# Kernel tuning notes

Measured on AMD Instinct MI355X. Metric: run time of the kernel, lower is better.

The kernel has to match this reference:

```python
import jax, jax.numpy as jnp
import numpy as np

N_NODES = 16384   # n_features in the torch code (graph nodes)
N_EDGES = 262144  # nnz of sparse Laplacian (avg degree 16)
K = 4             # receptive_field_k (Chebyshev order)
F_OUT = 32        # gconv_filter_size
BATCH = 256       # n_batch


def setup_inputs() -> dict:
    key = jax.random.key(0)
    k1, k2, k3, k4, k5, k6 = jax.random.split(key, 6)
    x = jax.random.normal(k1, (BATCH, N_NODES), dtype=jnp.float32)
    rows = jax.random.randint(k2, (N_EDGES,), 0, N_NODES)
    cols = jax.random.randint(k3, (N_EDGES,), 0, N_NODES)
    vals = jax.random.normal(k4, (N_EDGES,), dtype=jnp.float32) * 0.1
    bound = 1.0 / np.sqrt(K)  # kaiming-uniform-ish init bound, fan_in = K
    weight = jax.random.uniform(k5, (F_OUT, K), minval=-bound, maxval=bound, dtype=jnp.float32)
    bias = jax.random.uniform(k6, (F_OUT,), minval=-bound, maxval=bound, dtype=jnp.float32)
    return dict(x=x, vals=vals, rows=rows, cols=cols, weight=weight, bias=bias)


def _spmm(vals, rows, cols, xT):
    # sparse L @ xT with xT: (N, B); edge-wise gather then segment-sum scatter
    contrib = vals[:, None] * xT[cols]  # (E, B)
    return jax.ops.segment_sum(contrib, rows, num_segments=N_NODES)


def reference(x, vals, rows, cols, weight, bias):
    # Scaled Laplacian: Lhat = 2*L/lmax - I; normalized Laplacian has lmax=2 -> Lhat = L - I
    xT = x.T  # (N, B)

    def lhat(v):
        return _spmm(vals, rows, cols, v) - v

    # Chebyshev recurrence: T0 = x, T1 = Lhat x, Tk = 2 Lhat T_{k-1} - T_{k-2}
    t0 = xT
    t1 = lhat(t0)
    terms = [t0, t1]
    for _ in range(K - 2):
        terms.append(2.0 * lhat(terms[-1]) - terms[-2])
    xk = jnp.stack(terms, axis=0)  # (K, N, B)

    # original stacks (K, B, N), permutes (1,2,0) -> (B, N, K), reshape -> (B*N, K)
    feats = jnp.transpose(xk, (2, 1, 0)).reshape(BATCH * N_NODES, K)
    y = feats @ weight.T + bias  # F.linear
    return y.reshape(BATCH, N_NODES, F_OUT)
```

## Files before the change

### kernel.cpp

```cpp
#include <hip/hip_runtime.h>

#define N_NODES 16384
#define N_EDGES 262144
#define BATCH   256
#define F_OUT   32
#define K_ORD   4
#define NCHUNK  8
#define CHUNK   32
#define NPB     8

typedef float f32x4 __attribute__((ext_vector_type(4)));

__global__ void transpose_kernel(const float* __restrict__ x, float* __restrict__ xT) {
    __shared__ float tile[32][33];
    int tx = threadIdx.x;
    int ty = threadIdx.y;
    int n0 = blockIdx.x * 32;
    int b0 = blockIdx.y * 32;
#pragma unroll
    for (int j = 0; j < 4; ++j) {
        int b = b0 + ty + j * 8;
        int n = n0 + tx;
        tile[ty + j * 8][tx] = x[(size_t)b * N_NODES + n];
    }
    __syncthreads();
#pragma unroll
    for (int j = 0; j < 4; ++j) {
        int n = n0 + ty + j * 8;
        int b = b0 + tx;
        xT[(size_t)n * BATCH + b] = tile[tx][ty + j * 8];
    }
}

__global__ void hist_kernel(const int* __restrict__ rows, int* __restrict__ count) {
    int e = blockIdx.x * blockDim.x + threadIdx.x;
    if (e < N_EDGES) atomicAdd(&count[rows[e]], 1);
}

__global__ void scan_kernel(int* __restrict__ count, int* __restrict__ row_ptr) {
    __shared__ int part[256];
    int t = threadIdx.x;
    int base = t * 64;
    int loc[64];
    int s = 0;
#pragma unroll
    for (int i = 0; i < 64; ++i) { loc[i] = count[base + i]; s += loc[i]; }
    part[t] = s;
    __syncthreads();
    for (int d = 1; d < 256; d <<= 1) {
        int v = (t >= d) ? part[t - d] : 0;
        __syncthreads();
        part[t] += v;
        __syncthreads();
    }
    int off = part[t] - s;
#pragma unroll
    for (int i = 0; i < 64; ++i) {
        row_ptr[base + i] = off;
        count[base + i] = off;
        off += loc[i];
    }
    if (t == 255) row_ptr[N_NODES] = off;
}

__global__ void scatter_kernel(const int* __restrict__ rows, const int* __restrict__ cols,
                               const float* __restrict__ vals,
                               int* __restrict__ cursor,
                               int* __restrict__ csr_col, float* __restrict__ csr_val) {
    int e = blockIdx.x * blockDim.x + threadIdx.x;
    if (e < N_EDGES) {
        int r = rows[e];
        int pos = atomicAdd(&cursor[r], 1);
        csr_col[pos] = cols[e];
        csr_val[pos] = vals[e];
    }
}

__global__ void cheb_kernel(const float* __restrict__ in, const float* __restrict__ prev,
                            float* __restrict__ out,
                            const int* __restrict__ row_ptr,
                            const float* __restrict__ csr_val, const int* __restrict__ csr_col,
                            float c) {
    int chunk = blockIdx.x & (NCHUNK - 1);
    int ng    = blockIdx.x >> 3;
    int nsub  = threadIdx.x >> 5;
    int b     = chunk * CHUNK + (threadIdx.x & 31);
    int n     = ng * NPB + nsub;
    int beg = row_ptr[n], end = row_ptr[n + 1];
    float acc = 0.f;
    int e = beg;
    for (; e + 3 < end; e += 4) {
        int   c0 = csr_col[e],     c1 = csr_col[e + 1], c2 = csr_col[e + 2], c3 = csr_col[e + 3];
        float v0 = csr_val[e],     v1 = csr_val[e + 1], v2 = csr_val[e + 2], v3 = csr_val[e + 3];
        acc += v0 * in[(size_t)c0 * BATCH + b];
        acc += v1 * in[(size_t)c1 * BATCH + b];
        acc += v2 * in[(size_t)c2 * BATCH + b];
        acc += v3 * in[(size_t)c3 * BATCH + b];
    }
    for (; e < end; ++e)
        acc += csr_val[e] * in[(size_t)csr_col[e] * BATCH + b];
    size_t idx = (size_t)n * BATCH + b;
    float o = c * (acc - in[idx]);
    if (prev) o -= prev[idx];
    out[idx] = o;
}

__global__ void final_kernel(const float* __restrict__ t0, const float* __restrict__ t1,
                             const float* __restrict__ t2,
                             const int* __restrict__ row_ptr,
                             const float* __restrict__ csr_val, const int* __restrict__ csr_col,
                             const float* __restrict__ weight, const float* __restrict__ bias,
                             float* __restrict__ out) {
    __shared__ float w[F_OUT * K_ORD];
    __shared__ float bb[F_OUT];
    __shared__ f32x4 tval[NPB][CHUNK];
    int tid = threadIdx.x;
    if (tid < F_OUT * K_ORD) w[tid] = weight[tid];
    if (tid < F_OUT) bb[tid] = bias[tid];

    int chunk = blockIdx.x & (NCHUNK - 1);
    int ng    = blockIdx.x >> 3;
    {
        int nsub = tid >> 5;
        int bi   = tid & 31;
        int b    = chunk * CHUNK + bi;
        int n    = ng * NPB + nsub;
        int beg = row_ptr[n], end = row_ptr[n + 1];
        float acc = 0.f;
        int e = beg;
        for (; e + 3 < end; e += 4) {
            int   c0 = csr_col[e],     c1 = csr_col[e + 1], c2 = csr_col[e + 2], c3 = csr_col[e + 3];
            float v0 = csr_val[e],     v1 = csr_val[e + 1], v2 = csr_val[e + 2], v3 = csr_val[e + 3];
            acc += v0 * t2[(size_t)c0 * BATCH + b];
            acc += v1 * t2[(size_t)c1 * BATCH + b];
            acc += v2 * t2[(size_t)c2 * BATCH + b];
            acc += v3 * t2[(size_t)c3 * BATCH + b];
        }
        for (; e < end; ++e)
            acc += csr_val[e] * t2[(size_t)csr_col[e] * BATCH + b];

        size_t idx = (size_t)n * BATCH + b;
        float t2v = t2[idx];
        float t3v = 2.f * (acc - t2v) - t1[idx];
        tval[nsub][bi] = (f32x4){t0[idx], t1[idx], t2v, t3v};
    }
    __syncthreads();

    int f = (tid & 7) * 4;
    f32x4 w0 = *(const f32x4*)&w[(f + 0) * 4];
    f32x4 w1 = *(const f32x4*)&w[(f + 1) * 4];
    f32x4 w2 = *(const f32x4*)&w[(f + 2) * 4];
    f32x4 w3 = *(const f32x4*)&w[(f + 3) * 4];
    f32x4 b4 = *(const f32x4*)&bb[f];

    int nsub = (tid >> 3) & 7;
    int wv   = tid >> 6;
    size_t n = (size_t)(ng * NPB + nsub);
#pragma unroll
    for (int i = 0; i < 8; ++i) {
        int b_idx = i * 4 + wv;
        size_t b  = (size_t)(chunk * CHUNK + b_idx);
        f32x4 tv = tval[nsub][b_idx];
        f32x4 r;
        r.x = w0.x * tv.x + w0.y * tv.y + w0.z * tv.z + w0.w * tv.w + b4.x;
        r.y = w1.x * tv.x + w1.y * tv.y + w1.z * tv.z + w1.w * tv.w + b4.y;
        r.z = w2.x * tv.x + w2.y * tv.y + w2.z * tv.z + w2.w * tv.w + b4.z;
        r.w = w3.x * tv.x + w3.y * tv.y + w3.z * tv.z + w3.w * tv.w + b4.w;
        __builtin_nontemporal_store(r, (f32x4*)(out + (b * N_NODES + n) * F_OUT + f));
    }
}

extern "C" void kernel_launch(void* const* d_in, const int* in_sizes, int n_in,
                              void* d_out, int out_size, void* d_ws, size_t ws_size,
                              hipStream_t stream) {
    const float* x      = (const float*)d_in[0];
    const float* vals   = (const float*)d_in[1];
    const int*   rows   = (const int*)d_in[2];
    const int*   cols   = (const int*)d_in[3];
    const float* weight = (const float*)d_in[4];
    const float* bias   = (const float*)d_in[5];
    float* out = (float*)d_out;

    const size_t NB = (size_t)N_NODES * BATCH;
    float* xT      = (float*)d_ws;
    float* t1      = xT + NB;
    float* t2      = t1 + NB;
    int*   row_ptr = (int*)(t2 + NB);
    int*   cursor  = row_ptr + 16448;
    float* csr_val = (float*)(cursor + N_NODES);
    int*   csr_col = (int*)(csr_val + N_EDGES);

    (void)hipMemsetAsync(cursor, 0, N_NODES * sizeof(int), stream);

    transpose_kernel<<<dim3(N_NODES / 32, BATCH / 32), dim3(32, 8), 0, stream>>>(x, xT);
    hist_kernel<<<N_EDGES / 256, 256, 0, stream>>>(rows, cursor);
    scan_kernel<<<1, 256, 0, stream>>>(cursor, row_ptr);
    scatter_kernel<<<N_EDGES / 256, 256, 0, stream>>>(rows, cols, vals, cursor, csr_col, csr_val);

    const int GRID = (N_NODES / NPB) * NCHUNK;
    cheb_kernel<<<GRID, 256, 0, stream>>>(xT, nullptr, t1, row_ptr, csr_val, csr_col, 1.f);
    cheb_kernel<<<GRID, 256, 0, stream>>>(t1, xT, t2, row_ptr, csr_val, csr_col, 2.f);
    final_kernel<<<GRID, 256, 0, stream>>>(xT, t1, t2, row_ptr, csr_val, csr_col,
                                           weight, bias, out);
}
```

Before: 247.7 us.

## Gather SpMM operands in bf16 with packed col/val CSR and 2-wide batch lanes

Keeps bf16 shadow copies of each Chebyshev term and gathers neighbour rows from them, halving gather bytes. Column index and a bf16 edge value are packed into one 32-bit word, and each thread now handles two batch elements, with the chunk count halved to match. The self and previous terms stay in fp32. The cost is extra bf16 writes and lower accuracy in the sparse products, which may push results past the tolerance.

```diff
diff --git a/kernel.cpp b/kernel.cpp
--- a/kernel.cpp
+++ b/kernel.cpp
@@ -5,13 +5,23 @@
 #define BATCH   256
 #define F_OUT   32
 #define K_ORD   4
-#define NCHUNK  8
-#define CHUNK   32
+#define NCHUNK  4
+#define CHUNK   64
 #define NPB     8
 
 typedef float f32x4 __attribute__((ext_vector_type(4)));
-
-__global__ void transpose_kernel(const float* __restrict__ x, float* __restrict__ xT) {
+typedef float f32x2 __attribute__((ext_vector_type(2)));
+
+__device__ __forceinline__ unsigned short f2bf(float f) {
+    unsigned u = __float_as_uint(f);
+    return (unsigned short)((u + 0x7FFFu + ((u >> 16) & 1u)) >> 16);
+}
+__device__ __forceinline__ float bf2f(unsigned v) {
+    return __uint_as_float(v << 16);
+}
+
+__global__ void transpose_kernel(const float* __restrict__ x, float* __restrict__ xT,
+                                 unsigned short* __restrict__ xb) {
     __shared__ float tile[32][33];
     int tx = threadIdx.x;
     int ty = threadIdx.y;
@@ -28,7 +38,9 @@
     for (int j = 0; j < 4; ++j) {
         int n = n0 + ty + j * 8;
         int b = b0 + tx;
-        xT[(size_t)n * BATCH + b] = tile[tx][ty + j * 8];
+        float v = tile[tx][ty + j * 8];
+        xT[(size_t)n * BATCH + b] = v;
+        xb[(size_t)n * BATCH + b] = f2bf(v);
     }
 }
 
@@ -66,83 +78,105 @@
 __global__ void scatter_kernel(const int* __restrict__ rows, const int* __restrict__ cols,
                                const float* __restrict__ vals,
                                int* __restrict__ cursor,
-                               int* __restrict__ csr_col, float* __restrict__ csr_val) {
+                               unsigned* __restrict__ csrp) {
     int e = blockIdx.x * blockDim.x + threadIdx.x;
     if (e < N_EDGES) {
         int r = rows[e];
         int pos = atomicAdd(&cursor[r], 1);
-        csr_col[pos] = cols[e];
-        csr_val[pos] = vals[e];
-    }
-}
-
-__global__ void cheb_kernel(const float* __restrict__ in, const float* __restrict__ prev,
-                            float* __restrict__ out,
+        csrp[pos] = (unsigned)cols[e] | ((unsigned)f2bf(vals[e]) << 16);
+    }
+}
+
+__global__ void cheb_kernel(const float* __restrict__ in, const unsigned short* __restrict__ inb,
+                            const float* __restrict__ prev,
+                            float* __restrict__ out, unsigned short* __restrict__ outb,
                             const int* __restrict__ row_ptr,
-                            const float* __restrict__ csr_val, const int* __restrict__ csr_col,
-                            float c) {
+                            const unsigned* __restrict__ csrp, float c) {
     int chunk = blockIdx.x & (NCHUNK - 1);
-    int ng    = blockIdx.x >> 3;
+    int ng    = blockIdx.x >> 2;
     int nsub  = threadIdx.x >> 5;
-    int b     = chunk * CHUNK + (threadIdx.x & 31);
+    int b     = chunk * CHUNK + (threadIdx.x & 31) * 2;
     int n     = ng * NPB + nsub;
     int beg = row_ptr[n], end = row_ptr[n + 1];
-    float acc = 0.f;
+    f32x2 acc = (f32x2)(0.f);
     int e = beg;
     for (; e + 3 < end; e += 4) {
-        int   c0 = csr_col[e],     c1 = csr_col[e + 1], c2 = csr_col[e + 2], c3 = csr_col[e + 3];
-        float v0 = csr_val[e],     v1 = csr_val[e + 1], v2 = csr_val[e + 2], v3 = csr_val[e + 3];
-        acc += v0 * in[(size_t)c0 * BATCH + b];
-        acc += v1 * in[(size_t)c1 * BATCH + b];
-        acc += v2 * in[(size_t)c2 * BATCH + b];
-        acc += v3 * in[(size_t)c3 * BATCH + b];
-    }
-    for (; e < end; ++e)
-        acc += csr_val[e] * in[(size_t)csr_col[e] * BATCH + b];
+        unsigned p0 = csrp[e], p1 = csrp[e + 1], p2 = csrp[e + 2], p3 = csrp[e + 3];
+        unsigned g0 = *(const unsigned*)&inb[(size_t)(p0 & 0xFFFF) * BATCH + b];
+        unsigned g1 = *(const unsigned*)&inb[(size_t)(p1 & 0xFFFF) * BATCH + b];
+        unsigned g2 = *(const unsigned*)&inb[(size_t)(p2 & 0xFFFF) * BATCH + b];
+        unsigned g3 = *(const unsigned*)&inb[(size_t)(p3 & 0xFFFF) * BATCH + b];
+        float v0 = bf2f(p0 >> 16), v1 = bf2f(p1 >> 16), v2 = bf2f(p2 >> 16), v3 = bf2f(p3 >> 16);
+        acc.x += v0 * bf2f(g0 & 0xFFFF) + v1 * bf2f(g1 & 0xFFFF)
+               + v2 * bf2f(g2 & 0xFFFF) + v3 * bf2f(g3 & 0xFFFF);
+        acc.y += v0 * bf2f(g0 >> 16) + v1 * bf2f(g1 >> 16)
+               + v2 * bf2f(g2 >> 16) + v3 * bf2f(g3 >> 16);
+    }
+    for (; e < end; ++e) {
+        unsigned p = csrp[e];
+        unsigned g = *(const unsigned*)&inb[(size_t)(p & 0xFFFF) * BATCH + b];
+        float v = bf2f(p >> 16);
+        acc.x += v * bf2f(g & 0xFFFF);
+        acc.y += v * bf2f(g >> 16);
+    }
     size_t idx = (size_t)n * BATCH + b;
-    float o = c * (acc - in[idx]);
-    if (prev) o -= prev[idx];
-    out[idx] = o;
+    f32x2 self = *(const f32x2*)&in[idx];
+    f32x2 o = c * (acc - self);
+    if (prev) o -= *(const f32x2*)&prev[idx];
+    *(f32x2*)&out[idx] = o;
+    *(unsigned*)&outb[idx] = (unsigned)f2bf(o.x) | ((unsigned)f2bf(o.y) << 16);
 }
 
 __global__ void final_kernel(const float* __restrict__ t0, const float* __restrict__ t1,
-                             const float* __restrict__ t2,
+                             const float* __restrict__ t2, const unsigned short* __restrict__ t2b,
                              const int* __restrict__ row_ptr,
-                             const float* __restrict__ csr_val, const int* __restrict__ csr_col,
+                             const unsigned* __restrict__ csrp,
                              const float* __restrict__ weight, const float* __restrict__ bias,
                              float* __restrict__ out) {
     __shared__ float w[F_OUT * K_ORD];
     __shared__ float bb[F_OUT];
-    __shared__ f32x4 tval[NPB][CHUNK];
+    __shared__ f32x4 tval[NPB][CHUNK + 1];
     int tid = threadIdx.x;
     if (tid < F_OUT * K_ORD) w[tid] = weight[tid];
     if (tid < F_OUT) bb[tid] = bias[tid];
+    __syncthreads();
 
     int chunk = blockIdx.x & (NCHUNK - 1);
-    int ng    = blockIdx.x >> 3;
+    int ng    = blockIdx.x >> 2;
     {
         int nsub = tid >> 5;
-        int bi   = tid & 31;
+        int bi   = (tid & 31) * 2;
         int b    = chunk * CHUNK + bi;
         int n    = ng * NPB + nsub;
         int beg = row_ptr[n], end = row_ptr[n + 1];
-        float acc = 0.f;
+        f32x2 acc = (f32x2)(0.f);
         int e = beg;
         for (; e + 3 < end; e += 4) {
-            int   c0 = csr_col[e],     c1 = csr_col[e + 1], c2 = csr_col[e + 2], c3 = csr_col[e + 3];
-            float v0 = csr_val[e],     v1 = csr_val[e + 1], v2 = csr_val[e + 2], v3 = csr_val[e + 3];
-            acc += v0 * t2[(size_t)c0 * BATCH + b];
-            acc += v1 * t2[(size_t)c1 * BATCH + b];
-            acc += v2 * t2[(size_t)c2 * BATCH + b];
-            acc += v3 * t2[(size_t)c3 * BATCH + b];
+            unsigned p0 = csrp[e], p1 = csrp[e + 1], p2 = csrp[e + 2], p3 = csrp[e + 3];
+            unsigned g0 = *(const unsigned*)&t2b[(size_t)(p0 & 0xFFFF) * BATCH + b];
+            unsigned g1 = *(const unsigned*)&t2b[(size_t)(p1 & 0xFFFF) * BATCH + b];
+            unsigned g2 = *(const unsigned*)&t2b[(size_t)(p2 & 0xFFFF) * BATCH + b];
+            unsigned g3 = *(const unsigned*)&t2b[(size_t)(p3 & 0xFFFF) * BATCH + b];
+            float v0 = bf2f(p0 >> 16), v1 = bf2f(p1 >> 16), v2 = bf2f(p2 >> 16), v3 = bf2f(p3 >> 16);
+            acc.x += v0 * bf2f(g0 & 0xFFFF) + v1 * bf2f(g1 & 0xFFFF)
+                   + v2 * bf2f(g2 & 0xFFFF) + v3 * bf2f(g3 & 0xFFFF);
+            acc.y += v0 * bf2f(g0 >> 16) + v1 * bf2f(g1 >> 16)
+                   + v2 * bf2f(g2 >> 16) + v3 * bf2f(g3 >> 16);
         }
-        for (; e < end; ++e)
-            acc += csr_val[e] * t2[(size_t)csr_col[e] * BATCH + b];
-
+        for (; e < end; ++e) {
+            unsigned p = csrp[e];
+            unsigned g = *(const unsigned*)&t2b[(size_t)(p & 0xFFFF) * BATCH + b];
+            float v = bf2f(p >> 16);
+            acc.x += v * bf2f(g & 0xFFFF);
+            acc.y += v * bf2f(g >> 16);
+        }
         size_t idx = (size_t)n * BATCH + b;
-        float t2v = t2[idx];
-        float t3v = 2.f * (acc - t2v) - t1[idx];
-        tval[nsub][bi] = (f32x4){t0[idx], t1[idx], t2v, t3v};
+        f32x2 t2v = *(const f32x2*)&t2[idx];
+        f32x2 t1v = *(const f32x2*)&t1[idx];
+        f32x2 t0v = *(const f32x2*)&t0[idx];
+        f32x2 t3v = 2.f * (acc - t2v) - t1v;
+        tval[nsub][bi]     = (f32x4){t0v.x, t1v.x, t2v.x, t3v.x};
+        tval[nsub][bi + 1] = (f32x4){t0v.y, t1v.y, t2v.y, t3v.y};
     }
     __syncthreads();
 
@@ -152,12 +186,11 @@
     f32x4 w2 = *(const f32x4*)&w[(f + 2) * 4];
     f32x4 w3 = *(const f32x4*)&w[(f + 3) * 4];
     f32x4 b4 = *(const f32x4*)&bb[f];
-
     int nsub = (tid >> 3) & 7;
     int wv   = tid >> 6;
     size_t n = (size_t)(ng * NPB + nsub);
 #pragma unroll
-    for (int i = 0; i < 8; ++i) {
+    for (int i = 0; i < 16; ++i) {
         int b_idx = i * 4 + wv;
         size_t b  = (size_t)(chunk * CHUNK + b_idx);
         f32x4 tv = tval[nsub][b_idx];
@@ -182,24 +215,26 @@
     float* out = (float*)d_out;
 
     const size_t NB = (size_t)N_NODES * BATCH;
-    float* xT      = (float*)d_ws;
-    float* t1      = xT + NB;
-    float* t2      = t1 + NB;
-    int*   row_ptr = (int*)(t2 + NB);
-    int*   cursor  = row_ptr + 16448;
-    float* csr_val = (float*)(cursor + N_NODES);
-    int*   csr_col = (int*)(csr_val + N_EDGES);
+    float*          xT      = (float*)d_ws;
+    float*          t1      = xT + NB;
+    float*          t2      = t1 + NB;
+    unsigned short* xb      = (unsigned short*)(t2 + NB);
+    unsigned short* t1b     = xb + NB;
+    unsigned short* t2b     = t1b + NB;
+    int*            row_ptr = (int*)(t2b + NB);
+    int*            cursor  = row_ptr + 16448;
+    unsigned*       csrp    = (unsigned*)(cursor + N_NODES);
 
     (void)hipMemsetAsync(cursor, 0, N_NODES * sizeof(int), stream);
 
-    transpose_kernel<<<dim3(N_NODES / 32, BATCH / 32), dim3(32, 8), 0, stream>>>(x, xT);
+    transpose_kernel<<<dim3(N_NODES / 32, BATCH / 32), dim3(32, 8), 0, stream>>>(x, xT, xb);
     hist_kernel<<<N_EDGES / 256, 256, 0, stream>>>(rows, cursor);
     scan_kernel<<<1, 256, 0, stream>>>(cursor, row_ptr);
-    scatter_kernel<<<N_EDGES / 256, 256, 0, stream>>>(rows, cols, vals, cursor, csr_col, csr_val);
+    scatter_kernel<<<N_EDGES / 256, 256, 0, stream>>>(rows, cols, vals, cursor, csrp);
 
     const int GRID = (N_NODES / NPB) * NCHUNK;
-    cheb_kernel<<<GRID, 256, 0, stream>>>(xT, nullptr, t1, row_ptr, csr_val, csr_col, 1.f);
-    cheb_kernel<<<GRID, 256, 0, stream>>>(t1, xT, t2, row_ptr, csr_val, csr_col, 2.f);
-    final_kernel<<<GRID, 256, 0, stream>>>(xT, t1, t2, row_ptr, csr_val, csr_col,
+    cheb_kernel<<<GRID, 256, 0, stream>>>(xT, xb, nullptr, t1, t1b, row_ptr, csrp, 1.f);
+    cheb_kernel<<<GRID, 256, 0, stream>>>(t1, t1b, xT, t2, t2b, row_ptr, csrp, 2.f);
+    final_kernel<<<GRID, 256, 0, stream>>>(xT, t1, t2, t2b, row_ptr, csrp,
                                            weight, bias, out);
 }
```

After: 214.4 us. 1.16x faster.
